# Kernel optimization log

Hardware: AMD Instinct MI355X
Metric: run time of the kernel (lower is better)

The kernel has to match this reference:

```python
import jax, jax.numpy as jnp
import numpy as np

B, LD = 256, 64
NO, LO = 10240, 32
NM, LM = 81920, 16
EO, EM = 81920, 327680
E, HID, H, Dh, V = 128, 256, 8, 16, 10000


def masked_mean(tokens, table):
    # tokens: [N, L] int; pad id = 0
    emb = table[tokens]                            # [N, L, E]
    mask = (tokens != 0)
    s = jnp.sum(emb * mask[..., None].astype(emb.dtype), axis=1)
    lens = jnp.maximum(jnp.sum(mask, axis=1), 1).astype(emb.dtype)
    return s / lens[:, None]


def segment_softmax(scores, seg, num_segments):
    # scores: [E, ...]; softmax over entries sharing seg id (PyG softmax)
    m = jax.ops.segment_max(scores, seg, num_segments=num_segments)
    e = jnp.exp(scores - m[seg])
    s = jax.ops.segment_sum(e, seg, num_segments=num_segments)
    return e / (s[seg] + 1e-16)


def gcn_conv(x, W, b, src, dst, n):
    # PyG GCNConv: normalize=True, add_self_loops=True
    xw = x @ W
    loops = jnp.arange(n, dtype=src.dtype)
    s2 = jnp.concatenate([src, loops])
    d2 = jnp.concatenate([dst, loops])
    deg = jax.ops.segment_sum(jnp.ones_like(d2, dtype=x.dtype), d2, num_segments=n)
    dinv = deg ** -0.5  # deg >= 1 due to self loops
    norm = dinv[s2] * dinv[d2]
    out = jax.ops.segment_sum(xw[s2] * norm[:, None], d2, num_segments=n)
    return out + b


def transformer_conv(x, Wq, bq, Wk, bk, Wv, bv, Wskip, bskip, src, dst, n):
    q = (x @ Wq + bq).reshape(n, H, Dh)
    k = (x @ Wk + bk).reshape(n, H, Dh)
    v = (x @ Wv + bv).reshape(n, H, Dh)
    score = jnp.sum(q[dst] * k[src], axis=-1) / jnp.sqrt(jnp.asarray(Dh, x.dtype))  # [E, H]
    alpha = segment_softmax(score, dst, n)
    agg = jax.ops.segment_sum(alpha[:, :, None] * v[src], dst, num_segments=n)  # [n, H, Dh]
    return agg.reshape(n, H * Dh) + x @ Wskip + bskip


def global_attention(x, Wg, bg, seg, num_segments):
    gate = x @ Wg + bg                              # [N, 1]
    a = segment_softmax(gate, seg, num_segments)
    return jax.ops.segment_sum(a * x, seg, num_segments=num_segments)


def setup_inputs():
    key = jax.random.key(0)
    ks = jax.random.split(key, 20)
    sc = lambda k, shape: jax.random.normal(k, shape, dtype=jnp.float32) * 0.05
    inp = {
        "desc_tokens": jax.random.randint(ks[0], (B, LD), 0, V, dtype=jnp.int32),
        "x_tokens": jax.random.randint(ks[1], (NO, LO), 0, V, dtype=jnp.int32),
        "mini_tokens": jax.random.randint(ks[2], (NM, LM), 0, V, dtype=jnp.int32),
        "src": jax.random.randint(ks[3], (EO,), 0, NO, dtype=jnp.int32),
        "dst": jax.random.randint(ks[4], (EO,), 0, NO, dtype=jnp.int32),
        "mini_src": jax.random.randint(ks[5], (EM,), 0, NM, dtype=jnp.int32),
        "mini_dst": jax.random.randint(ks[6], (EM,), 0, NM, dtype=jnp.int32),
        "mini_batch": (jnp.arange(NM, dtype=jnp.int32) // (NM // NO)),
        "node_batch": (jnp.arange(NO, dtype=jnp.int32) // (NO // B)),
        "desc_table": sc(ks[7], (V, E)),
        "code_table": sc(ks[8], (V, E)),
        "code_table2": sc(ks[9], (V, E)),
        "Wq": sc(ks[10], (E, H * Dh)), "bq": jnp.zeros((H * Dh,), jnp.float32),
        "Wk": sc(ks[11], (E, H * Dh)), "bk": jnp.zeros((H * Dh,), jnp.float32),
        "Wv": sc(ks[12], (E, H * Dh)), "bv": jnp.zeros((H * Dh,), jnp.float32),
        "Wskip": sc(ks[13], (E, H * Dh)), "bskip": jnp.zeros((H * Dh,), jnp.float32),
        "W2": sc(ks[14], (E, HID)), "b2": jnp.zeros((HID,), jnp.float32),
        "W3": sc(ks[15], (HID, E)), "b3": jnp.zeros((E,), jnp.float32),
        "Wg": sc(ks[16], (E, 1)), "bg": jnp.zeros((1,), jnp.float32),
    }
    return inp


def reference(desc_tokens, x_tokens, mini_tokens, src, dst, mini_src, mini_dst,
              mini_batch, node_batch, desc_table, code_table, code_table2,
              Wq, bq, Wk, bk, Wv, bv, Wskip, bskip, W2, b2, W3, b3, Wg, bg):
    # encode_desc: embedding + masked mean pool -> [B, E]
    h_n = masked_mean(desc_tokens, desc_table)
    # encode_code_graph
    stmt_emb = masked_mean(x_tokens, code_table2)          # [NO, E]
    mini_emb = masked_mean(mini_tokens, code_table)        # [NM, E]
    mini_hidden = transformer_conv(mini_emb, Wq, bq, Wk, bk, Wv, bv,
                                   Wskip, bskip, mini_src, mini_dst, NM)
    mini_fn = global_attention(mini_hidden, Wg, bg, mini_batch, NO)  # [NO, E]
    mini_fn = (mini_fn + stmt_emb) * 0.5
    h = jax.nn.relu(gcn_conv(mini_fn, W2, b2, src, dst, NO))
    final_stmt = gcn_conv(h, W3, b3, src, dst, NO)
    fn_repr = global_attention(final_stmt, Wg, bg, node_batch, B)    # [B, E]
    # cosine similarity (torch eps=1e-8 clamps each norm)
    na = jnp.maximum(jnp.linalg.norm(fn_repr, axis=-1), 1e-8)
    nb = jnp.maximum(jnp.linalg.norm(h_n, axis=-1), 1e-8)
    return jnp.sum(fn_repr * h_n, axis=-1) / (na * nb)
```

## Files before the change

kernel.cpp:

```cpp
#include <hip/hip_runtime.h>
#include <hip/hip_bf16.h>
#include <math.h>

#define BB   256
#define LDE  64
#define NO   10240
#define LO   32
#define NM   81920
#define LM   16
#define EO   81920
#define EM   327680
#define ED   128
#define HIDD 256
#define NH   8
#define DH   16
#define VV   10000

static inline int nblk(long long n, int b) { return (int)((n + b - 1) / b); }

typedef __attribute__((ext_vector_type(8))) short short8;
typedef __attribute__((ext_vector_type(4))) float f32x4;

static __device__ __forceinline__ unsigned short bf16_rne(float f) {
  unsigned u = __float_as_uint(f);
  return (unsigned short)((u + 0x7fffu + ((u >> 16) & 1u)) >> 16);
}
static __device__ __forceinline__ float bf16_to_f(unsigned short h) {
  return __uint_as_float(((unsigned)h) << 16);
}
static __device__ __forceinline__ float4 b4f(ushort4 h) {
  return make_float4(bf16_to_f(h.x), bf16_to_f(h.y), bf16_to_f(h.z), bf16_to_f(h.w));
}
static __device__ __forceinline__ ushort4 f4b(float4 v) {
  return make_ushort4(bf16_rne(v.x), bf16_rne(v.y), bf16_rne(v.z), bf16_rne(v.w));
}

struct WC { const float* W; int K, M; short8* hi; short8* lo; int base; };
struct WC6 { WC w[6]; };
#define TBLK (2 * VV * ED / 4 / 256)
#define ZBLK ((NM + NO) / 256)
__global__ void __launch_bounds__(256)
conv_all_k(WC6 wc, const float* __restrict__ t1, unsigned short* __restrict__ o1,
           const float* __restrict__ t2, unsigned short* __restrict__ o2,
           int* __restrict__ hist) {
  if (blockIdx.x < 64) {
    int g = blockIdx.x * 256 + threadIdx.x;
    int wi = 0;
    #pragma unroll
    for (int i = 1; i < 6; ++i) if (g >= wc.w[i].base) wi = i;
    const WC c = wc.w[wi];
    int idx = g - c.base;
    int lane = idx & 63;
    int nt = (idx >> 6) % (c.M / 16);
    int kb = (idx >> 6) / (c.M / 16);
    int n = nt * 16 + (lane & 15);
    int k0 = kb * 32 + ((lane >> 4) << 3);
    short8 h, l;
    #pragma unroll
    for (int j = 0; j < 8; ++j) {
      float v = c.W[(size_t)(k0 + j) * c.M + n];
      unsigned short hb = bf16_rne(v);
      h[j] = (short)hb;
      l[j] = (short)bf16_rne(v - bf16_to_f(hb));
    }
    c.hi[idx] = h; c.lo[idx] = l;
  } else if (blockIdx.x < 64 + TBLK) {
    int q = (blockIdx.x - 64) * 256 + threadIdx.x;
    const int NT = VV * ED / 4;
    if (q < NT) {
      float4 v = *(const float4*)(t1 + (size_t)q * 4);
      *(ushort4*)(o1 + (size_t)q * 4) = f4b(v);
    } else if (q < 2 * NT) {
      int q2 = q - NT;
      float4 v = *(const float4*)(t2 + (size_t)q2 * 4);
      *(ushort4*)(o2 + (size_t)q2 * 4) = f4b(v);
    }
  } else {
    int i = (blockIdx.x - 64 - TBLK) * 256 + threadIdx.x;
    if (i < NM + NO) hist[i] = 0;
  }
}

template<int L>
static __device__ __forceinline__ void embed_body_f(const int* __restrict__ tokens,
                                                    const float* __restrict__ table,
                                                    float* __restrict__ out, int blk) {
  const int r = threadIdx.x >> 5, lane = threadIdx.x & 31;
  const int n0 = blk * 8;
  __shared__ int toks[8][L];
  for (int i = threadIdx.x; i < 8 * L; i += 256)
    toks[i / L][i % L] = tokens[(size_t)n0 * L + i];
  __syncthreads();
  float4 acc = make_float4(0.f, 0.f, 0.f, 0.f);
  int cnt = 0;
  #pragma unroll
  for (int l = 0; l < L; ++l) {
    int t = toks[r][l];
    float4 v = *(const float4*)(table + (size_t)t * ED + lane * 4);
    float msk = (t != 0) ? 1.f : 0.f;
    cnt += (t != 0);
    acc.x = fmaf(msk, v.x, acc.x); acc.y = fmaf(msk, v.y, acc.y);
    acc.z = fmaf(msk, v.z, acc.z); acc.w = fmaf(msk, v.w, acc.w);
  }
  float inv = 1.f / (float)(cnt > 0 ? cnt : 1);
  acc.x *= inv; acc.y *= inv; acc.z *= inv; acc.w *= inv;
  *(float4*)(out + (size_t)(n0 + r) * ED + lane * 4) = acc;
}

template<int L>
static __device__ __forceinline__ void embed_body16(const int* __restrict__ tokens,
                                                    const unsigned short* __restrict__ table,
                                                    unsigned short* __restrict__ out, int blk) {
  const int r = threadIdx.x >> 4, lane = threadIdx.x & 15;
  const int n0 = blk * 16;
  __shared__ int toks[16][L];
  for (int i = threadIdx.x; i < 16 * L; i += 256)
    toks[i / L][i % L] = tokens[(size_t)n0 * L + i];
  __syncthreads();
  float acc[8] = {};
  int cnt = 0;
  #pragma unroll
  for (int l = 0; l < L; ++l) {
    int t = toks[r][l];
    short8 v = *(const short8*)(table + (size_t)t * ED + lane * 8);
    float msk = (t != 0) ? 1.f : 0.f;
    cnt += (t != 0);
    #pragma unroll
    for (int j = 0; j < 8; ++j)
      acc[j] = fmaf(msk, bf16_to_f((unsigned short)v[j]), acc[j]);
  }
  float inv = 1.f / (float)(cnt > 0 ? cnt : 1);
  short8 o;
  #pragma unroll
  for (int j = 0; j < 8; ++j) o[j] = (short)bf16_rne(acc[j] * inv);
  *(short8*)(out + (size_t)(n0 + r) * ED + lane * 8) = o;
}

__global__ void __launch_bounds__(256)
embed_all_k(const int* __restrict__ desc_tokens, const float* __restrict__ desc_table,
            float* __restrict__ h_n,
            const int* __restrict__ x_tokens, const unsigned short* __restrict__ ctab2,
            unsigned short* __restrict__ stmt,
            const int* __restrict__ mini_tokens, const unsigned short* __restrict__ ctab,
            unsigned short* __restrict__ miniE) {
  int b = blockIdx.x;
  if (b < BB / 8) embed_body_f<LDE>(desc_tokens, desc_table, h_n, b);
  else if (b < BB / 8 + NO / 16) embed_body16<LO>(x_tokens, ctab2, stmt, b - BB / 8);
  else embed_body16<LM>(mini_tokens, ctab, miniE, b - BB / 8 - NO / 16);
}

struct QDesc { const short8* bh; const float* bias; unsigned short* C;
               int rstride; int gmul; int goff; };
struct QDesc4 { QDesc d[4]; };

__global__ void __launch_bounds__(512)
mgemm_qkvs8_k(const unsigned short* __restrict__ Ab, QDesc4 g4) {
  const int id = blockIdx.x;
  const int mat = (id >> 3) & 3;
  const int rowb = (id & 7) | ((id >> 5) << 3);
  const QDesc d = g4.d[mat];
  const int n0 = rowb * 128;
  const int tid = threadIdx.x;
  const int w = tid >> 6, lane = tid & 63;
  const int wm = (w & 3) * 2;
  const int wn = (w >> 2) * 4;
  const int r = lane & 15, qd = lane >> 4;
  f32x4 acc[2][4];
  #pragma unroll
  for (int i = 0; i < 2; ++i)
    #pragma unroll
    for (int j = 0; j < 4; ++j) acc[i][j] = (f32x4){0.f, 0.f, 0.f, 0.f};
  #pragma unroll
  for (int kb = 0; kb < 4; ++kb) {
    short8 bh[4];
    #pragma unroll
    for (int j = 0; j < 4; ++j)
      bh[j] = d.bh[((size_t)kb * 8 + wn + j) * 64 + lane];
    short8 a[2];
    #pragma unroll
    for (int i = 0; i < 2; ++i)
      a[i] = *(const short8*)(Ab + (size_t)(n0 + (wm + i) * 16 + r) * ED + kb * 32 + qd * 8);
    #pragma unroll
    for (int i = 0; i < 2; ++i)
      #pragma unroll
      for (int j = 0; j < 4; ++j)
        acc[i][j] = __builtin_amdgcn_mfma_f32_16x16x32_bf16(bh[j], a[i], acc[i][j], 0, 0, 0);
  }
  #pragma unroll
  for (int i = 0; i < 2; ++i)
    #pragma unroll
    for (int j = 0; j < 4; ++j) {
      const int node = n0 + (wm + i) * 16 + r;
      const int colb = (wn + j) * 16 + qd * 4;
      const float4 bv = *(const float4*)(d.bias + colb);
      const int cidx = ((wn + j) * 4 + qd) * d.gmul + d.goff;
      ushort4 o;
      o.x = bf16_rne(acc[i][j][0] + bv.x);
      o.y = bf16_rne(acc[i][j][1] + bv.y);
      o.z = bf16_rne(acc[i][j][2] + bv.z);
      o.w = bf16_rne(acc[i][j][3] + bv.w);
      *(ushort4*)(d.C + (size_t)node * d.rstride + cidx) = o;
    }
}

template<bool RELU>
__global__ void __launch_bounds__(512)
mgemm_b_k(const unsigned short* __restrict__ Ab, const short8* __restrict__ Bh,
          const float* __restrict__ bias, unsigned short* __restrict__ C,
          int K, int M) {
  const int bn0 = blockIdx.x * 128;
  const int n0 = blockIdx.y * 128;
  const int tid = threadIdx.x;
  const int w = tid >> 6, lane = tid & 63;
  const int wm = (w & 3) * 2, wn = (w >> 2) * 4;
  const int r = lane & 15, qd = lane >> 4;
  const int NTm = M / 16;
  f32x4 acc[2][4];
  #pragma unroll
  for (int i = 0; i < 2; ++i)
    #pragma unroll
    for (int j = 0; j < 4; ++j) acc[i][j] = (f32x4){0.f, 0.f, 0.f, 0.f};
  const int kbn = K / 32;
  for (int kb = 0; kb < kbn; ++kb) {
    short8 bh[4];
    #pragma unroll
    for (int j = 0; j < 4; ++j)
      bh[j] = Bh[((size_t)kb * NTm + (bn0 >> 4) + wn + j) * 64 + lane];
    short8 a[2];
    #pragma unroll
    for (int i = 0; i < 2; ++i)
      a[i] = *(const short8*)(Ab + (size_t)(n0 + (wm + i) * 16 + r) * K + kb * 32 + qd * 8);
    #pragma unroll
    for (int i = 0; i < 2; ++i)
      #pragma unroll
      for (int j = 0; j < 4; ++j)
        acc[i][j] = __builtin_amdgcn_mfma_f32_16x16x32_bf16(bh[j], a[i], acc[i][j], 0, 0, 0);
  }
  #pragma unroll
  for (int i = 0; i < 2; ++i)
    #pragma unroll
    for (int j = 0; j < 4; ++j) {
      const int node = n0 + (wm + i) * 16 + r;
      const int colb = bn0 + (wn + j) * 16 + qd * 4;
      float4 bv = bias ? *(const float4*)(bias + colb) : make_float4(0.f, 0.f, 0.f, 0.f);
      float v0 = acc[i][j][0] + bv.x;
      float v1 = acc[i][j][1] + bv.y;
      float v2 = acc[i][j][2] + bv.z;
      float v3 = acc[i][j][3] + bv.w;
      if (RELU) {
        v0 = fmaxf(v0, 0.f); v1 = fmaxf(v1, 0.f);
        v2 = fmaxf(v2, 0.f); v3 = fmaxf(v3, 0.f);
      }
      ushort4 o = make_ushort4(bf16_rne(v0), bf16_rne(v1), bf16_rne(v2), bf16_rne(v3));
      *(ushort4*)(C + (size_t)node * M + colb) = o;
    }
}

__global__ void hist2_k(const int* __restrict__ dm, int* __restrict__ hm,
                        const int* __restrict__ dd, int* __restrict__ ho) {
  int e = blockIdx.x * 256 + threadIdx.x;
  if (e < EM) atomicAdd(&hm[dm[e]], 1);
  else { int e2 = e - EM; if (e2 < EO) atomicAdd(&ho[dd[e2]], 1); }
}
__global__ void chunk_sum_k(const int* __restrict__ hist, int* __restrict__ partials, int N) {
  __shared__ int sd[256];
  int i = blockIdx.x * 256 + threadIdx.x;
  sd[threadIdx.x] = (i < N) ? hist[i] : 0;
  __syncthreads();
  for (int s = 128; s > 0; s >>= 1) {
    if (threadIdx.x < s) sd[threadIdx.x] += sd[threadIdx.x + s];
    __syncthreads();
  }
  if (threadIdx.x == 0) partials[blockIdx.x] = sd[0];
}
__global__ void scan_partials2_k(int* __restrict__ p) {
  __shared__ int sd[512];
  int base = (blockIdx.x == 0) ? 0 : NM / 256;
  int B    = (blockIdx.x == 0) ? NM / 256 : NO / 256;
  int t = threadIdx.x;
  int v = (t < B) ? p[base + t] : 0;
  sd[t] = v; __syncthreads();
  for (int off = 1; off < 512; off <<= 1) {
    int a = (t >= off) ? sd[t - off] : 0;
    __syncthreads();
    sd[t] += a;
    __syncthreads();
  }
  if (t < B) p[base + t] = sd[t] - v;
}
__global__ void scan_final2_k(const int* __restrict__ hist, const int* __restrict__ partials,
                              int* __restrict__ offsm, int* __restrict__ curm,
                              int* __restrict__ offso, int* __restrict__ curo,
                              float* __restrict__ dinv) {
  __shared__ int sd[256];
  int i = blockIdx.x * 256 + threadIdx.x;
  int v = hist[i];
  sd[threadIdx.x] = v; __syncthreads();
  for (int off = 1; off < 256; off <<= 1) {
    int a = (threadIdx.x >= off) ? sd[threadIdx.x - off] : 0;
    __syncthreads();
    sd[threadIdx.x] += a;
    __syncthreads();
  }
  int excl = sd[threadIdx.x] - v + partials[blockIdx.x];
  if (i < NM) {
    offsm[i] = excl; curm[i] = excl;
    if (i == NM - 1) offsm[NM] = excl + v;
  } else {
    int i2 = i - NM;
    offso[i2] = excl; curo[i2] = excl;
    if (i2 == NO - 1) offso[NO] = excl + v;
    dinv[i2] = 1.f / sqrtf(1.f + (float)v);
  }
}
__global__ void scatter2_k(const int* __restrict__ sm, const int* __restrict__ dm,
                           int* __restrict__ cm, int* __restrict__ km,
                           const int* __restrict__ so, const int* __restrict__ dd,
                           int* __restrict__ co, int* __restrict__ ko) {
  int e = blockIdx.x * 256 + threadIdx.x;
  if (e < EM) {
    int pos = atomicAdd(&cm[dm[e]], 1);
    km[pos] = sm[e];
  } else {
    int e2 = e - EM;
    if (e2 < EO) {
      int pos = atomicAdd(&co[dd[e2]], 1);
      ko[pos] = so[e2];
    }
  }
}

__global__ void __launch_bounds__(128)
attn_fused_k(unsigned short* qh, const unsigned short* __restrict__ kv,
             const unsigned short* __restrict__ skip,
             const int* __restrict__ offs, const int* __restrict__ csr,
             const float* __restrict__ Wg, const float* __restrict__ bg,
             float* __restrict__ gateOut) {
  const int g = threadIdx.x >> 5, lane = threadIdx.x & 31;
  const int n = blockIdx.x * 4 + g;
  float4 q = b4f(*(const ushort4*)(qh + (size_t)n * ED + lane * 4));
  int lo = offs[n], hi = offs[n + 1];
  float4 O = make_float4(0.f, 0.f, 0.f, 0.f);
  float m = -INFINITY, l = 0.f;
  for (int base = lo; base < hi; base += 4) {
    int rem = hi - base;
    int sidx[4];
    #pragma unroll
    for (int i = 0; i < 4; ++i) sidx[i] = (i < rem) ? csr[base + i] : 0;
    short8 kvr[4];
    #pragma unroll
    for (int i = 0; i < 4; ++i)
      kvr[i] = *(const short8*)(kv + (size_t)sidx[i] * (2 * ED) + lane * 8);
    #pragma unroll
    for (int i = 0; i < 4; ++i) {
      float4 kt = make_float4(bf16_to_f((unsigned short)kvr[i][0]),
                              bf16_to_f((unsigned short)kvr[i][1]),
                              bf16_to_f((unsigned short)kvr[i][2]),
                              bf16_to_f((unsigned short)kvr[i][3]));
      float4 vt = make_float4(bf16_to_f((unsigned short)kvr[i][4]),
                              bf16_to_f((unsigned short)kvr[i][5]),
                              bf16_to_f((unsigned short)kvr[i][6]),
                              bf16_to_f((unsigned short)kvr[i][7]));
      float p = q.x * kt.x + q.y * kt.y + q.z * kt.z + q.w * kt.w;
      p += __shfl_xor(p, 1, 64);
      p += __shfl_xor(p, 2, 64);
      float sc = (i < rem) ? p * 0.25f : -INFINITY;
      float mn = fmaxf(m, sc);
      float scale = __expf(m - mn);
      float pe = __expf(sc - mn);
      l = l * scale + pe;
      O.x = O.x * scale + pe * vt.x; O.y = O.y * scale + pe * vt.y;
      O.z = O.z * scale + pe * vt.z; O.w = O.w * scale + pe * vt.w;
      m = mn;
    }
  }
  float inv = 1.f / (l + 1e-16f);
  float4 sk = b4f(*(const ushort4*)(skip + (size_t)n * ED + lane * 4));
  float4 out = make_float4(O.x * inv + sk.x, O.y * inv + sk.y,
                           O.z * inv + sk.z, O.w * inv + sk.w);
  *(ushort4*)(qh + (size_t)n * ED + lane * 4) = f4b(out);
  float4 wg = *(const float4*)(Wg + lane * 4);
  float ps = out.x * wg.x + out.y * wg.y + out.z * wg.z + out.w * wg.w;
  #pragma unroll
  for (int o = 1; o <= 16; o <<= 1) ps += __shfl_xor(ps, o, 64);
  if (lane == 0) gateOut[n] = ps + bg[0];
}

__global__ void __launch_bounds__(256)
gcn_gather_b_k(const unsigned short* __restrict__ x, const float* __restrict__ dinv,
               const int* __restrict__ offs, const int* __restrict__ csr,
               const float* __restrict__ bias, unsigned short* __restrict__ out,
               const float* __restrict__ Wg, const float* __restrict__ bg,
               float* __restrict__ gateOut) {
  const int wv = threadIdx.x >> 6, lane = threadIdx.x & 63;
  const int half = lane >> 5, cl = lane & 31;
  const int n = blockIdx.x * 4 + wv;
  float di = dinv[n];
  float4 acc = make_float4(0.f, 0.f, 0.f, 0.f);
  if (half == 0) {
    float4 xs = b4f(*(const ushort4*)(x + (size_t)n * ED + cl * 4));
    float w0 = di * di;
    acc = make_float4(w0 * xs.x, w0 * xs.y, w0 * xs.z, w0 * xs.w);
  }
  int lo = offs[n], hi = offs[n + 1];
  for (int base = lo; base < hi; base += 8) {
    int sidx[4]; bool ok[4];
    #pragma unroll
    for (int i = 0; i < 4; ++i) {
      int e = base + 2 * i + half;
      ok[i] = e < hi;
      sidx[i] = ok[i] ? csr[e] : 0;
    }
    float dw[4];
    #pragma unroll
    for (int i = 0; i < 4; ++i) dw[i] = ok[i] ? di * dinv[sidx[i]] : 0.f;
    ushort4 vr[4];
    #pragma unroll
    for (int i = 0; i < 4; ++i)
      vr[i] = *(const ushort4*)(x + (size_t)sidx[i] * ED + cl * 4);
    #pragma unroll
    for (int i = 0; i < 4; ++i) {
      float4 v = b4f(vr[i]);
      acc.x = fmaf(dw[i], v.x, acc.x); acc.y = fmaf(dw[i], v.y, acc.y);
      acc.z = fmaf(dw[i], v.z, acc.z); acc.w = fmaf(dw[i], v.w, acc.w);
    }
  }
  acc.x += __shfl_xor(acc.x, 32, 64); acc.y += __shfl_xor(acc.y, 32, 64);
  acc.z += __shfl_xor(acc.z, 32, 64); acc.w += __shfl_xor(acc.w, 32, 64);
  if (bias) {
    float4 b4 = *(const float4*)(bias + cl * 4);
    acc.x += b4.x; acc.y += b4.y; acc.z += b4.z; acc.w += b4.w;
  }
  if (half == 0)
    *(ushort4*)(out + (size_t)n * ED + cl * 4) = f4b(acc);
  if (gateOut) {
    float4 wg = *(const float4*)(Wg + cl * 4);
    float ps = acc.x * wg.x + acc.y * wg.y + acc.z * wg.z + acc.w * wg.w;
    #pragma unroll
    for (int o = 1; o <= 16; o <<= 1) ps += __shfl_xor(ps, o, 64);
    if (lane == 0) gateOut[n] = ps + bg[0];
  }
}

static __device__ __forceinline__ int lower_bound_d(const int* a, int n, int key) {
  int lo = 0, hi = n;
  while (lo < hi) { int mid = (lo + hi) >> 1; if (a[mid] < key) lo = mid + 1; else hi = mid; }
  return lo;
}
__global__ void __launch_bounds__(128)
gattn_comb_b_k(const unsigned short* __restrict__ xv, const float* __restrict__ gate,
               const int* __restrict__ seg, int Ntot,
               const unsigned short* __restrict__ other, unsigned short* __restrict__ out) {
  const int g = threadIdx.x >> 5, lane = threadIdx.x & 31;
  const int n = blockIdx.x * 4 + g;
  __shared__ int sh[4][2];
  if (lane == 0) {
    sh[g][0] = lower_bound_d(seg, Ntot, n);
    sh[g][1] = lower_bound_d(seg, Ntot, n + 1);
  }
  __syncthreads();
  int lo = sh[g][0], hi = sh[g][1];
  float m = -INFINITY;
  for (int j = lo; j < hi; ++j) m = fmaxf(m, gate[j]);
  float ssum = 0.f;
  for (int j = lo; j < hi; ++j) ssum += __expf(gate[j] - m);
  float inv = 1.f / (ssum + 1e-16f);
  float4 acc = make_float4(0.f, 0.f, 0.f, 0.f);
  for (int j = lo; j < hi; ++j) {
    float a = __expf(gate[j] - m) * inv;
    float4 v = b4f(*(const ushort4*)(xv + (size_t)j * ED + lane * 4));
    acc.x = fmaf(a, v.x, acc.x); acc.y = fmaf(a, v.y, acc.y);
    acc.z = fmaf(a, v.z, acc.z); acc.w = fmaf(a, v.w, acc.w);
  }
  float4 o4 = b4f(*(const ushort4*)(other + (size_t)n * ED + lane * 4));
  acc.x = (acc.x + o4.x) * 0.5f; acc.y = (acc.y + o4.y) * 0.5f;
  acc.z = (acc.z + o4.z) * 0.5f; acc.w = (acc.w + o4.w) * 0.5f;
  *(ushort4*)(out + (size_t)n * ED + lane * 4) = f4b(acc);
}

__global__ void __launch_bounds__(128)
gattn_cos_k(const unsigned short* __restrict__ x, const float* __restrict__ gate,
            const int* __restrict__ seg, int Ntot,
            const float* __restrict__ hn, float* __restrict__ outp) {
  const int g = threadIdx.x >> 5, lane = threadIdx.x & 31;
  const int n = blockIdx.x * 4 + g;
  __shared__ int sh[4][2];
  if (lane == 0) {
    sh[g][0] = lower_bound_d(seg, Ntot, n);
    sh[g][1] = lower_bound_d(seg, Ntot, n + 1);
  }
  __syncthreads();
  int lo = sh[g][0], hi = sh[g][1];
  float m = -INFINITY;
  for (int j = lo; j < hi; ++j) m = fmaxf(m, gate[j]);
  float ssum = 0.f;
  for (int j = lo; j < hi; ++j) ssum += __expf(gate[j] - m);
  float inv = 1.f / (ssum + 1e-16f);
  float4 acc = make_float4(0.f, 0.f, 0.f, 0.f);
  for (int j = lo; j < hi; ++j) {
    float a = __expf(gate[j] - m) * inv;
    float4 v = b4f(*(const ushort4*)(x + (size_t)j * ED + lane * 4));
    acc.x = fmaf(a, v.x, acc.x); acc.y = fmaf(a, v.y, acc.y);
    acc.z = fmaf(a, v.z, acc.z); acc.w = fmaf(a, v.w, acc.w);
  }
  float4 hv = *(const float4*)(hn + (size_t)n * ED + lane * 4);
  float dot = acc.x * hv.x + acc.y * hv.y + acc.z * hv.z + acc.w * hv.w;
  float na  = acc.x * acc.x + acc.y * acc.y + acc.z * acc.z + acc.w * acc.w;
  float nb  = hv.x * hv.x + hv.y * hv.y + hv.z * hv.z + hv.w * hv.w;
  #pragma unroll
  for (int o = 1; o <= 16; o <<= 1) {
    dot += __shfl_xor(dot, o, 64);
    na  += __shfl_xor(na,  o, 64);
    nb  += __shfl_xor(nb,  o, 64);
  }
  if (lane == 0)
    outp[n] = dot / (fmaxf(sqrtf(na), 1e-8f) * fmaxf(sqrtf(nb), 1e-8f));
}

constexpr size_t OFF_HN    = 0;
constexpr size_t OFF_STMT  = OFF_HN    + (size_t)BB * ED;
constexpr size_t OFF_A     = OFF_STMT  + (size_t)NO * ED;
constexpr size_t OFF_QHID  = OFF_A     + (size_t)NM * ED;
constexpr size_t OFF_CT    = OFF_QHID  + (size_t)NM * ED / 2;
constexpr size_t OFF_K     = OFF_QHID  + (size_t)NM * ED;
constexpr size_t OFF_V     = OFF_K     + (size_t)NM * ED;
constexpr size_t T0        = OFF_V     + (size_t)NM * ED;
constexpr size_t OFF_GATE  = T0;
constexpr size_t OFF_GATE2 = OFF_GATE  + (size_t)NM;
constexpr size_t OFF_DINV  = OFF_GATE2 + (size_t)NO;
constexpr size_t OFF_HISTM = OFF_DINV  + (size_t)NO;
constexpr size_t OFF_HISTO = OFF_HISTM + (size_t)NM;
constexpr size_t OFF_OFFSM = OFF_HISTO + (size_t)NO;
constexpr size_t OFF_CURM  = OFF_OFFSM + (size_t)NM + 1;
constexpr size_t OFF_CSRM  = OFF_CURM  + (size_t)NM;
constexpr size_t OFF_OFFSO = OFF_CSRM  + (size_t)EM;
constexpr size_t OFF_CURO  = OFF_OFFSO + (size_t)NO + 1;
constexpr size_t OFF_CSRO  = OFF_CURO  + (size_t)NO;
constexpr size_t OFF_PART  = OFF_CSRO  + (size_t)EO;
constexpr size_t OFF_WFHI  = OFF_PART  + 512;
constexpr size_t OFF_WFLO  = OFF_WFHI  + 65536;
constexpr size_t WO_Q  = 0, WO_K = 2048, WO_V = 4096, WO_S = 6144, WO_W2 = 8192, WO_W3 = 12288;
constexpr size_t OFF_MFN   = OFF_A;
constexpr size_t OFF_AGG   = OFF_MFN   + (size_t)NO * ED;
constexpr size_t OFF_H     = OFF_AGG   + (size_t)NO * ED;
constexpr size_t OFF_T     = OFF_H     + (size_t)NO * HIDD;
constexpr size_t OFF_FIN   = OFF_T     + (size_t)NO * ED;

extern "C" void kernel_launch(void* const* d_in, const int* in_sizes, int n_in,
                              void* d_out, int out_size, void* d_ws, size_t ws_size,
                              hipStream_t stream) {
  const int* desc_tokens = (const int*)d_in[0];
  const int* x_tokens    = (const int*)d_in[1];
  const int* mini_tokens = (const int*)d_in[2];
  const int* src         = (const int*)d_in[3];
  const int* dst         = (const int*)d_in[4];
  const int* mini_src    = (const int*)d_in[5];
  const int* mini_dst    = (const int*)d_in[6];
  const int* mini_batch  = (const int*)d_in[7];
  const int* node_batch  = (const int*)d_in[8];
  const float* desc_table  = (const float*)d_in[9];
  const float* code_table  = (const float*)d_in[10];
  const float* code_table2 = (const float*)d_in[11];
  const float* Wq = (const float*)d_in[12]; const float* bq = (const float*)d_in[13];
  const float* Wk = (const float*)d_in[14]; const float* bk = (const float*)d_in[15];
  const float* Wv = (const float*)d_in[16]; const float* bv = (const float*)d_in[17];
  const float* Wskip = (const float*)d_in[18]; const float* bskip = (const float*)d_in[19];
  const float* W2 = (const float*)d_in[20]; const float* b2 = (const float*)d_in[21];
  const float* W3 = (const float*)d_in[22]; const float* b3 = (const float*)d_in[23];
  const float* Wg = (const float*)d_in[24]; const float* bg = (const float*)d_in[25];

  float* ws = (float*)d_ws;
  float* h_n   = ws + OFF_HN;
  unsigned short* stmt_b  = (unsigned short*)(ws + OFF_STMT);
  unsigned short* miniE_b = (unsigned short*)(ws + OFF_A);
  unsigned short* qhid_b = (unsigned short*)(ws + OFF_QHID);
  unsigned short* ctab_b  = (unsigned short*)(ws + OFF_CT);
  unsigned short* ctab2_b = (unsigned short*)(ws + OFF_CT + (size_t)VV * ED / 2);
  unsigned short* kv_b   = (unsigned short*)(ws + OFF_K);
  unsigned short* skip_b = (unsigned short*)(ws + OFF_V);
  float* gate  = ws + OFF_GATE;
  float* gate2 = ws + OFF_GATE2;
  float* dinv  = ws + OFF_DINV;
  int* histm = (int*)(ws + OFF_HISTM);
  int* histo = (int*)(ws + OFF_HISTO);
  int* offsm = (int*)(ws + OFF_OFFSM);
  int* curm  = (int*)(ws + OFF_CURM);
  int* csrm  = (int*)(ws + OFF_CSRM);
  int* offso = (int*)(ws + OFF_OFFSO);
  int* curo  = (int*)(ws + OFF_CURO);
  int* csro  = (int*)(ws + OFF_CSRO);
  int* part  = (int*)(ws + OFF_PART);
  short8* wfhi = (short8*)(ws + OFF_WFHI);
  short8* wflo = (short8*)(ws + OFF_WFLO);
  unsigned short* mini_fn_b = (unsigned short*)(ws + OFF_MFN);
  unsigned short* aggb_b    = (unsigned short*)(ws + OFF_AGG);
  unsigned short* hbuf_b    = (unsigned short*)(ws + OFF_H);
  unsigned short* tbuf_b    = (unsigned short*)(ws + OFF_T);
  unsigned short* finalS_b  = (unsigned short*)(ws + OFF_FIN);
  float* outp    = (float*)d_out;

  WC6 wc;
  wc.w[0] = {Wq,    ED,   ED,   wfhi + WO_Q,  wflo + WO_Q,  (int)WO_Q};
  wc.w[1] = {Wk,    ED,   ED,   wfhi + WO_K,  wflo + WO_K,  (int)WO_K};
  wc.w[2] = {Wv,    ED,   ED,   wfhi + WO_V,  wflo + WO_V,  (int)WO_V};
  wc.w[3] = {Wskip, ED,   ED,   wfhi + WO_S,  wflo + WO_S,  (int)WO_S};
  wc.w[4] = {W2,    ED,   HIDD, wfhi + WO_W2, wflo + WO_W2, (int)WO_W2};
  wc.w[5] = {W3,    HIDD, ED,   wfhi + WO_W3, wflo + WO_W3, (int)WO_W3};
  conv_all_k<<<64 + TBLK + ZBLK, 256, 0, stream>>>(
      wc, code_table, ctab_b, code_table2, ctab2_b, histm);

  hist2_k<<<nblk(EM + EO, 256), 256, 0, stream>>>(mini_dst, histm, dst, histo);
  chunk_sum_k<<<(NM + NO) / 256, 256, 0, stream>>>(histm, part, NM + NO);
  scan_partials2_k<<<2, 512, 0, stream>>>(part);
  scan_final2_k<<<(NM + NO) / 256, 256, 0, stream>>>(histm, part, offsm, curm,
                                                     offso, curo, dinv);
  scatter2_k<<<nblk(EM + EO, 256), 256, 0, stream>>>(mini_src, mini_dst, curm, csrm,
                                                     src, dst, curo, csro);

  embed_all_k<<<BB / 8 + NO / 16 + NM / 16, 256, 0, stream>>>(
      desc_tokens, desc_table, h_n, x_tokens, ctab2_b, stmt_b,
      mini_tokens, ctab_b, miniE_b);

  QDesc4 g4;
  g4.d[0] = {wfhi + WO_Q, bq,    qhid_b, ED,     4, 0};
  g4.d[1] = {wfhi + WO_K, bk,    kv_b,   2 * ED, 8, 0};
  g4.d[2] = {wfhi + WO_V, bv,    kv_b,   2 * ED, 8, 4};
  g4.d[3] = {wfhi + WO_S, bskip, skip_b, ED,     4, 0};
  mgemm_qkvs8_k<<<4 * (NM / 128), 512, 0, stream>>>(miniE_b, g4);

  attn_fused_k<<<NM / 4, 128, 0, stream>>>(qhid_b, kv_b, skip_b,
                                           offsm, csrm, Wg, bg, gate);

  gattn_comb_b_k<<<NO / 4, 128, 0, stream>>>(qhid_b, gate, mini_batch, NM,
                                             stmt_b, mini_fn_b);

  gcn_gather_b_k<<<NO / 4, 256, 0, stream>>>(mini_fn_b, dinv, offso, csro, nullptr,
                                             aggb_b, nullptr, nullptr, nullptr);
  { dim3 g(HIDD / 128, NO / 128);
    mgemm_b_k<true><<<g, 512, 0, stream>>>(aggb_b, wfhi + WO_W2, b2, hbuf_b, ED, HIDD); }

  { dim3 g(1, NO / 128);
    mgemm_b_k<false><<<g, 512, 0, stream>>>(hbuf_b, wfhi + WO_W3, nullptr, tbuf_b, HIDD, ED); }
  gcn_gather_b_k<<<NO / 4, 256, 0, stream>>>(tbuf_b, dinv, offso, csro, b3, finalS_b,
                                             Wg, bg, gate2);

  gattn_cos_k<<<BB / 4, 128, 0, stream>>>(finalS_b, gate2, node_batch, NO, h_n, outp);
}
```

Baseline: 351.1 us.

## Merge Q/K/V/skip projections into one interleaved 512-wide output buffer

```diff
diff --git a/kernel.cpp b/kernel.cpp
--- a/kernel.cpp
+++ b/kernel.cpp
@@ -35,49 +35,73 @@
   return make_ushort4(bf16_rne(v.x), bf16_rne(v.y), bf16_rne(v.z), bf16_rne(v.w));
 }
 
-struct WC { const float* W; int K, M; short8* hi; short8* lo; int base; };
-struct WC6 { WC w[6]; };
+struct ConvArgs {
+  const float *Wq, *Wk, *Wv, *Ws, *W2, *W3;
+  const float *bq, *bk, *bv, *bs;
+  short8* frag;
+  float* bias512;
+  const float* t1; unsigned short* o1;
+  const float* t2; unsigned short* o2;
+  int* hist;
+};
 #define TBLK (2 * VV * ED / 4 / 256)
 #define ZBLK ((NM + NO) / 256)
 __global__ void __launch_bounds__(256)
-conv_all_k(WC6 wc, const float* __restrict__ t1, unsigned short* __restrict__ o1,
-           const float* __restrict__ t2, unsigned short* __restrict__ o2,
-           int* __restrict__ hist) {
-  if (blockIdx.x < 64) {
-    int g = blockIdx.x * 256 + threadIdx.x;
-    int wi = 0;
-    #pragma unroll
-    for (int i = 1; i < 6; ++i) if (g >= wc.w[i].base) wi = i;
-    const WC c = wc.w[wi];
-    int idx = g - c.base;
-    int lane = idx & 63;
-    int nt = (idx >> 6) % (c.M / 16);
-    int kb = (idx >> 6) / (c.M / 16);
+conv_all_k(ConvArgs A) {
+  int b = blockIdx.x;
+  if (b < 32) {
+    int g = b * 256 + threadIdx.x;
+    int lane = g & 63, fid = g >> 6;
+    int nt = fid & 31, kb = fid >> 5;
+    int c = nt * 16 + (lane & 15);
+    int k0 = kb * 32 + ((lane >> 4) << 3);
+    const float* wp; int cm;
+    if (c < 128)      { wp = A.Wq; cm = c; }
+    else if (c < 384) { int u = c - 128, t = u & 7;
+                        wp = (t < 4) ? A.Wk : A.Wv; cm = (u >> 3) * 4 + (t & 3); }
+    else              { wp = A.Ws; cm = c - 384; }
+    short8 h;
+    #pragma unroll
+    for (int j = 0; j < 8; ++j)
+      h[j] = (short)bf16_rne(wp[(size_t)(k0 + j) * 128 + cm]);
+    A.frag[g] = h;
+  } else if (b < 64) {
+    int g = (b - 32) * 256 + threadIdx.x;
+    const float* wp; int M, dstbase, gg;
+    if (g < 4096) { wp = A.W2; M = 256; dstbase = 8192;  gg = g; }
+    else          { wp = A.W3; M = 128; dstbase = 12288; gg = g - 4096; }
+    int lane = gg & 63, fid = gg >> 6;
+    int nt = fid % (M / 16), kb = fid / (M / 16);
     int n = nt * 16 + (lane & 15);
     int k0 = kb * 32 + ((lane >> 4) << 3);
-    short8 h, l;
-    #pragma unroll
-    for (int j = 0; j < 8; ++j) {
-      float v = c.W[(size_t)(k0 + j) * c.M + n];
-      unsigned short hb = bf16_rne(v);
-      h[j] = (short)hb;
-      l[j] = (short)bf16_rne(v - bf16_to_f(hb));
-    }
-    c.hi[idx] = h; c.lo[idx] = l;
-  } else if (blockIdx.x < 64 + TBLK) {
-    int q = (blockIdx.x - 64) * 256 + threadIdx.x;
+    short8 h;
+    #pragma unroll
+    for (int j = 0; j < 8; ++j)
+      h[j] = (short)bf16_rne(wp[(size_t)(k0 + j) * M + n]);
+    A.frag[dstbase + gg] = h;
+  } else if (b < 64 + TBLK) {
+    int q = (b - 64) * 256 + threadIdx.x;
     const int NT = VV * ED / 4;
     if (q < NT) {
-      float4 v = *(const float4*)(t1 + (size_t)q * 4);
-      *(ushort4*)(o1 + (size_t)q * 4) = f4b(v);
+      float4 v = *(const float4*)(A.t1 + (size_t)q * 4);
+      *(ushort4*)(A.o1 + (size_t)q * 4) = f4b(v);
     } else if (q < 2 * NT) {
       int q2 = q - NT;
-      float4 v = *(const float4*)(t2 + (size_t)q2 * 4);
-      *(ushort4*)(o2 + (size_t)q2 * 4) = f4b(v);
-    }
+      float4 v = *(const float4*)(A.t2 + (size_t)q2 * 4);
+      *(ushort4*)(A.o2 + (size_t)q2 * 4) = f4b(v);
+    }
+  } else if (b < 64 + TBLK + ZBLK) {
+    int i = (b - 64 - TBLK) * 256 + threadIdx.x;
+    if (i < NM + NO) A.hist[i] = 0;
   } else {
-    int i = (blockIdx.x - 64 - TBLK) * 256 + threadIdx.x;
-    if (i < NM + NO) hist[i] = 0;
+    for (int c = threadIdx.x; c < 512; c += 256) {
+      float v;
+      if (c < 128)      v = A.bq[c];
+      else if (c < 384) { int u = c - 128, t = u & 7;
+                          v = (t < 4) ? A.bk[(u >> 3) * 4 + t] : A.bv[(u >> 3) * 4 + (t & 3)]; }
+      else              v = A.bs[c - 384];
+      A.bias512[c] = v;
+    }
   }
 }
 
@@ -149,58 +173,52 @@
   else embed_body16<LM>(mini_tokens, ctab, miniE, b - BB / 8 - NO / 16);
 }
 
-struct QDesc { const short8* bh; const float* bias; unsigned short* C;
-               int rstride; int gmul; int goff; };
-struct QDesc4 { QDesc d[4]; };
-
 __global__ void __launch_bounds__(512)
-mgemm_qkvs8_k(const unsigned short* __restrict__ Ab, QDesc4 g4) {
+qkvs_merged_k(const unsigned short* __restrict__ Ab, const short8* __restrict__ Wf,
+              const float* __restrict__ bias512, unsigned short* __restrict__ out) {
   const int id = blockIdx.x;
-  const int mat = (id >> 3) & 3;
-  const int rowb = (id & 7) | ((id >> 5) << 3);
-  const QDesc d = g4.d[mat];
-  const int n0 = rowb * 128;
+  const int blk = (id & 7) * 80 + (id >> 3);
+  const int n0 = blk * 128;
   const int tid = threadIdx.x;
   const int w = tid >> 6, lane = tid & 63;
-  const int wm = (w & 3) * 2;
-  const int wn = (w >> 2) * 4;
   const int r = lane & 15, qd = lane >> 4;
-  f32x4 acc[2][4];
-  #pragma unroll
-  for (int i = 0; i < 2; ++i)
-    #pragma unroll
-    for (int j = 0; j < 4; ++j) acc[i][j] = (f32x4){0.f, 0.f, 0.f, 0.f};
-  #pragma unroll
-  for (int kb = 0; kb < 4; ++kb) {
-    short8 bh[4];
-    #pragma unroll
-    for (int j = 0; j < 4; ++j)
-      bh[j] = d.bh[((size_t)kb * 8 + wn + j) * 64 + lane];
-    short8 a[2];
-    #pragma unroll
-    for (int i = 0; i < 2; ++i)
-      a[i] = *(const short8*)(Ab + (size_t)(n0 + (wm + i) * 16 + r) * ED + kb * 32 + qd * 8);
-    #pragma unroll
-    for (int i = 0; i < 2; ++i)
+  const int node = n0 + w * 16 + r;
+  __shared__ unsigned short lds[8 * 16 * 128];
+  char* myl = (char*)(lds + w * 2048);
+
+  short8 a[4];
+  #pragma unroll
+  for (int kb = 0; kb < 4; ++kb)
+    a[kb] = *(const short8*)(Ab + (size_t)node * ED + kb * 32 + qd * 8);
+
+  #pragma unroll
+  for (int ch = 0; ch < 4; ++ch) {
+    #pragma unroll 4
+    for (int jl = 0; jl < 8; ++jl) {
+      const int cf = ch * 8 + jl;
+      f32x4 acc = (f32x4){0.f, 0.f, 0.f, 0.f};
       #pragma unroll
-      for (int j = 0; j < 4; ++j)
-        acc[i][j] = __builtin_amdgcn_mfma_f32_16x16x32_bf16(bh[j], a[i], acc[i][j], 0, 0, 0);
-  }
-  #pragma unroll
-  for (int i = 0; i < 2; ++i)
-    #pragma unroll
-    for (int j = 0; j < 4; ++j) {
-      const int node = n0 + (wm + i) * 16 + r;
-      const int colb = (wn + j) * 16 + qd * 4;
-      const float4 bv = *(const float4*)(d.bias + colb);
-      const int cidx = ((wn + j) * 4 + qd) * d.gmul + d.goff;
+      for (int kb = 0; kb < 4; ++kb) {
+        short8 wf = Wf[((size_t)(kb * 32 + cf)) * 64 + lane];
+        acc = __builtin_amdgcn_mfma_f32_16x16x32_bf16(wf, a[kb], acc, 0, 0, 0);
+      }
+      const int colb = cf * 16 + qd * 4;
+      const float4 bv = *(const float4*)(bias512 + colb);
       ushort4 o;
-      o.x = bf16_rne(acc[i][j][0] + bv.x);
-      o.y = bf16_rne(acc[i][j][1] + bv.y);
-      o.z = bf16_rne(acc[i][j][2] + bv.z);
-      o.w = bf16_rne(acc[i][j][3] + bv.w);
-      *(ushort4*)(d.C + (size_t)node * d.rstride + cidx) = o;
-    }
+      o.x = bf16_rne(acc[0] + bv.x);
+      o.y = bf16_rne(acc[1] + bv.y);
+      o.z = bf16_rne(acc[2] + bv.z);
+      o.w = bf16_rne(acc[3] + bv.w);
+      *(ushort4*)(myl + r * 256 + (((jl * 32) ^ ((r & 7) << 5)) + qd * 8)) = o;
+    }
+    #pragma unroll
+    for (int t = 0; t < 4; ++t) {
+      const int rr = t * 4 + qd;
+      const int o16 = (lane & 15) * 16;
+      short8 v = *(const short8*)(myl + rr * 256 + (o16 ^ ((rr & 7) << 5)));
+      *(short8*)(out + (size_t)(n0 + w * 16 + rr) * 512 + ch * 128 + (lane & 15) * 8) = v;
+    }
+  }
 }
 
 template<bool RELU>
@@ -331,14 +349,13 @@
 }
 
 __global__ void __launch_bounds__(128)
-attn_fused_k(unsigned short* qh, const unsigned short* __restrict__ kv,
-             const unsigned short* __restrict__ skip,
+attn_fused_k(unsigned short* buf,
              const int* __restrict__ offs, const int* __restrict__ csr,
              const float* __restrict__ Wg, const float* __restrict__ bg,
              float* __restrict__ gateOut) {
   const int g = threadIdx.x >> 5, lane = threadIdx.x & 31;
   const int n = blockIdx.x * 4 + g;
-  float4 q = b4f(*(const ushort4*)(qh + (size_t)n * ED + lane * 4));
+  float4 q = b4f(*(const ushort4*)(buf + (size_t)n * 512 + lane * 4));
   int lo = offs[n], hi = offs[n + 1];
   float4 O = make_float4(0.f, 0.f, 0.f, 0.f);
   float m = -INFINITY, l = 0.f;
@@ -350,7 +367,7 @@
     short8 kvr[4];
     #pragma unroll
     for (int i = 0; i < 4; ++i)
-      kvr[i] = *(const short8*)(kv + (size_t)sidx[i] * (2 * ED) + lane * 8);
+      kvr[i] = *(const short8*)(buf + (size_t)sidx[i] * 512 + 128 + lane * 8);
     #pragma unroll
     for (int i = 0; i < 4; ++i) {
       float4 kt = make_float4(bf16_to_f((unsigned short)kvr[i][0]),
@@ -375,10 +392,10 @@
     }
   }
   float inv = 1.f / (l + 1e-16f);
-  float4 sk = b4f(*(const ushort4*)(skip + (size_t)n * ED + lane * 4));
+  float4 sk = b4f(*(const ushort4*)(buf + (size_t)n * 512 + 384 + lane * 4));
   float4 out = make_float4(O.x * inv + sk.x, O.y * inv + sk.y,
                            O.z * inv + sk.z, O.w * inv + sk.w);
-  *(ushort4*)(qh + (size_t)n * ED + lane * 4) = f4b(out);
+  *(ushort4*)(buf + (size_t)n * 512 + lane * 4) = f4b(out);
   float4 wg = *(const float4*)(Wg + lane * 4);
   float ps = out.x * wg.x + out.y * wg.y + out.z * wg.z + out.w * wg.w;
   #pragma unroll
@@ -468,7 +485,7 @@
   float4 acc = make_float4(0.f, 0.f, 0.f, 0.f);
   for (int j = lo; j < hi; ++j) {
     float a = __expf(gate[j] - m) * inv;
-    float4 v = b4f(*(const ushort4*)(xv + (size_t)j * ED + lane * 4));
+    float4 v = b4f(*(const ushort4*)(xv + (size_t)j * 512 + lane * 4));
     acc.x = fmaf(a, v.x, acc.x); acc.y = fmaf(a, v.y, acc.y);
     acc.z = fmaf(a, v.z, acc.z); acc.w = fmaf(a, v.w, acc.w);
   }
@@ -520,11 +537,9 @@
 constexpr size_t OFF_HN    = 0;
 constexpr size_t OFF_STMT  = OFF_HN    + (size_t)BB * ED;
 constexpr size_t OFF_A     = OFF_STMT  + (size_t)NO * ED;
-constexpr size_t OFF_QHID  = OFF_A     + (size_t)NM * ED;
-constexpr size_t OFF_CT    = OFF_QHID  + (size_t)NM * ED / 2;
-constexpr size_t OFF_K     = OFF_QHID  + (size_t)NM * ED;
-constexpr size_t OFF_V     = OFF_K     + (size_t)NM * ED;
-constexpr size_t T0        = OFF_V     + (size_t)NM * ED;
+constexpr size_t OFF_CT    = OFF_A     + (size_t)NM * ED;
+constexpr size_t OFF_QKVS  = OFF_CT    + (size_t)VV * ED;
+constexpr size_t T0        = OFF_QKVS  + (size_t)NM * 256;
 constexpr size_t OFF_GATE  = T0;
 constexpr size_t OFF_GATE2 = OFF_GATE  + (size_t)NM;
 constexpr size_t OFF_DINV  = OFF_GATE2 + (size_t)NO;
@@ -537,9 +552,8 @@
 constexpr size_t OFF_CURO  = OFF_OFFSO + (size_t)NO + 1;
 constexpr size_t OFF_CSRO  = OFF_CURO  + (size_t)NO;
 constexpr size_t OFF_PART  = OFF_CSRO  + (size_t)EO;
-constexpr size_t OFF_WFHI  = OFF_PART  + 512;
-constexpr size_t OFF_WFLO  = OFF_WFHI  + 65536;
-constexpr size_t WO_Q  = 0, WO_K = 2048, WO_V = 4096, WO_S = 6144, WO_W2 = 8192, WO_W3 = 12288;
+constexpr size_t OFF_B512  = OFF_PART  + 512;
+constexpr size_t OFF_WFHI  = OFF_B512  + 512;
 constexpr size_t OFF_MFN   = OFF_A;
 constexpr size_t OFF_AGG   = OFF_MFN   + (size_t)NO * ED;
 constexpr size_t OFF_H     = OFF_AGG   + (size_t)NO * ED;
@@ -573,11 +587,9 @@
   float* h_n   = ws + OFF_HN;
   unsigned short* stmt_b  = (unsigned short*)(ws + OFF_STMT);
   unsigned short* miniE_b = (unsigned short*)(ws + OFF_A);
-  unsigned short* qhid_b = (unsigned short*)(ws + OFF_QHID);
   unsigned short* ctab_b  = (unsigned short*)(ws + OFF_CT);
-  unsigned short* ctab2_b = (unsigned short*)(ws + OFF_CT + (size_t)VV * ED / 2);
-  unsigned short* kv_b   = (unsigned short*)(ws + OFF_K);
-  unsigned short* skip_b = (unsigned short*)(ws + OFF_V);
+  unsigned short* ctab2_b = ctab_b + (size_t)VV * ED;
+  unsigned short* qkvs_b  = (unsigned short*)(ws + OFF_QKVS);
   float* gate  = ws + OFF_GATE;
   float* gate2 = ws + OFF_GATE2;
   float* dinv  = ws + OFF_DINV;
@@ -590,8 +602,8 @@
   int* curo  = (int*)(ws + OFF_CURO);
   int* csro  = (int*)(ws + OFF_CSRO);
   int* part  = (int*)(ws + OFF_PART);
-  short8* wfhi = (short8*)(ws + OFF_WFHI);
-  short8* wflo = (short8*)(ws + OFF_WFLO);
+  float* bias512 = ws + OFF_B512;
+  short8* wfrag = (short8*)(ws + OFF_WFHI);
   unsigned short* mini_fn_b = (unsigned short*)(ws + OFF_MFN);
   unsigned short* aggb_b    = (unsigned short*)(ws + OFF_AGG);
   unsigned short* hbuf_b    = (unsigned short*)(ws + OFF_H);
@@ -599,15 +611,14 @@
   unsigned short* finalS_b  = (unsigned short*)(ws + OFF_FIN);
   float* outp    = (float*)d_out;
 
-  WC6 wc;
-  wc.w[0] = {Wq,    ED,   ED,   wfhi + WO_Q,  wflo + WO_Q,  (int)WO_Q};
-  wc.w[1] = {Wk,    ED,   ED,   wfhi + WO_K,  wflo + WO_K,  (int)WO_K};
-  wc.w[2] = {Wv,    ED,   ED,   wfhi + WO_V,  wflo + WO_V,  (int)WO_V};
-  wc.w[3] = {Wskip, ED,   ED,   wfhi + WO_S,  wflo + WO_S,  (int)WO_S};
-  wc.w[4] = {W2,    ED,   HIDD, wfhi + WO_W2, wflo + WO_W2, (int)WO_W2};
-  wc.w[5] = {W3,    HIDD, ED,   wfhi + WO_W3, wflo + WO_W3, (int)WO_W3};
-  conv_all_k<<<64 + TBLK + ZBLK, 256, 0, stream>>>(
-      wc, code_table, ctab_b, code_table2, ctab2_b, histm);
+  ConvArgs ca;
+  ca.Wq = Wq; ca.Wk = Wk; ca.Wv = Wv; ca.Ws = Wskip; ca.W2 = W2; ca.W3 = W3;
+  ca.bq = bq; ca.bk = bk; ca.bv = bv; ca.bs = bskip;
+  ca.frag = wfrag; ca.bias512 = bias512;
+  ca.t1 = code_table;  ca.o1 = ctab_b;
+  ca.t2 = code_table2; ca.o2 = ctab2_b;
+  ca.hist = histm;
+  conv_all_k<<<64 + TBLK + ZBLK + 1, 256, 0, stream>>>(ca);
 
   hist2_k<<<nblk(EM + EO, 256), 256, 0, stream>>>(mini_dst, histm, dst, histo);
   chunk_sum_k<<<(NM + NO) / 256, 256, 0, stream>>>(histm, part, NM + NO);
@@ -621,26 +632,20 @@
       desc_tokens, desc_table, h_n, x_tokens, ctab2_b, stmt_b,
       mini_tokens, ctab_b, miniE_b);
 
-  QDesc4 g4;
-  g4.d[0] = {wfhi + WO_Q, bq,    qhid_b, ED,     4, 0};
-  g4.d[1] = {wfhi + WO_K, bk,    kv_b,   2 * ED, 8, 0};
-  g4.d[2] = {wfhi + WO_V, bv,    kv_b,   2 * ED, 8, 4};
-  g4.d[3] = {wfhi + WO_S, bskip, skip_b, ED,     4, 0};
-  mgemm_qkvs8_k<<<4 * (NM / 128), 512, 0, stream>>>(miniE_b, g4);
-
-  attn_fused_k<<<NM / 4, 128, 0, stream>>>(qhid_b, kv_b, skip_b,
-                                           offsm, csrm, Wg, bg, gate);
-
-  gattn_comb_b_k<<<NO / 4, 128, 0, stream>>>(qhid_b, gate, mini_batch, NM,
+  qkvs_merged_k<<<NM / 128, 512, 0, stream>>>(miniE_b, wfrag, bias512, qkvs_b);
+
+  attn_fused_k<<<NM / 4, 128, 0, stream>>>(qkvs_b, offsm, csrm, Wg, bg, gate);
+
+  gattn_comb_b_k<<<NO / 4, 128, 0, stream>>>(qkvs_b, gate, mini_batch, NM,
                                              stmt_b, mini_fn_b);
 
   gcn_gather_b_k<<<NO / 4, 256, 0, stream>>>(mini_fn_b, dinv, offso, csro, nullptr,
                                              aggb_b, nullptr, nullptr, nullptr);
   { dim3 g(HIDD / 128, NO / 128);
-    mgemm_b_k<true><<<g, 512, 0, stream>>>(aggb_b, wfhi + WO_W2, b2, hbuf_b, ED, HIDD); }
+    mgemm_b_k<true><<<g, 512, 0, stream>>>(aggb_b, wfrag + 8192, b2, hbuf_b, ED, HIDD); }
 
   { dim3 g(1, NO / 128);
-    mgemm_b_k<false><<<g, 512, 0, stream>>>(hbuf_b, wfhi + WO_W3, nullptr, tbuf_b, HIDD, ED); }
+    mgemm_b_k<false><<<g, 512, 0, stream>>>(hbuf_b, wfrag + 12288, nullptr, tbuf_b, HIDD, ED); }
   gcn_gather_b_k<<<NO / 4, 256, 0, stream>>>(tbuf_b, dinv, offso, csro, b3, finalS_b,
                                              Wg, bg, gate2);
 
```

Result: faster. 342.5 us (-2.5%).
